# Kernel tuning notes

Hardware: AMD Instinct MI355X
Metric: run time of the kernel (lower is better)

The kernel has to match this reference:

```python
import jax, jax.numpy as jnp
import numpy as np

EPS = 1e-7

def safe_divide(num, den):
    safe_den = jnp.where(jnp.abs(den) > EPS, den, jnp.sign(den) * EPS)
    return num / safe_den

def mlp(x, W1, b1, W2, b2):
    return jnp.tanh(x @ W1 + b1) @ W2 + b2

B, L, C, H, T = 16384, 256, 512, 1024, 16

def setup_inputs() -> dict:
    key = jax.random.key(0)
    ks = jax.random.split(key, 12)
    s = 0.05
    z = jax.random.normal(ks[0], (B, 2 * L + 1), dtype=jnp.float32)
    ctx = jax.random.normal(ks[1], (B, T, C), dtype=jnp.float32)
    ts = jnp.arange(T, dtype=jnp.float32) * 0.1  # sorted time knots
    t = jnp.float32(0.75)                        # solver query time
    inverse_mass = jnp.ones((1, L), dtype=jnp.float32)
    # fixed diffusion = sqrt(2*gamma/beta), gamma=1, beta=1/3 -> sqrt(6)
    diffusion = jnp.full((1, L), np.sqrt(6.0), dtype=jnp.float32)
    # control_network: Linear(2L+C -> H), tanh, Linear(H -> L)
    Wc1 = jax.random.normal(ks[2], (2 * L + C, H), dtype=jnp.float32) * s
    bc1 = jnp.zeros((H,), dtype=jnp.float32)
    Wc2 = jax.random.normal(ks[3], (H, L), dtype=jnp.float32) * s
    bc2 = jnp.zeros((L,), dtype=jnp.float32)
    # h_net (prior drift): Linear(2L -> H), tanh, Linear(H -> L)
    Wh1 = jax.random.normal(ks[4], (2 * L, H), dtype=jnp.float32) * s
    bh1 = jnp.zeros((H,), dtype=jnp.float32)
    Wh2 = jax.random.normal(ks[5], (H, L), dtype=jnp.float32) * s
    bh2 = jnp.zeros((L,), dtype=jnp.float32)
    return {"z": z, "ts": ts, "t": t, "ctx": ctx,
            "inverse_mass": inverse_mass, "diffusion": diffusion,
            "Wc1": Wc1, "bc1": bc1, "Wc2": Wc2, "bc2": bc2,
            "Wh1": Wh1, "bh1": bh1, "Wh2": Wh2, "bh2": bh2}

def reference(z, ts, t, ctx, inverse_mass, diffusion,
              Wc1, bc1, Wc2, bc2, Wh1, bh1, Wh2, bh2):
    # f_and_g_absolute: one drift/diffusion evaluation of the second-order latent SDE
    pm = z[..., :-1]                      # [B, 2L] position+momentum
    momentum = pm[..., pm.shape[-1] // 2:]  # [B, L]
    # context lookup via searchsorted(right) clamped to last knot
    i = jnp.minimum(jnp.searchsorted(ts, t, side='right'), ts.shape[0] - 1)
    position_drift = inverse_mass * momentum                      # [B, L]
    prior_momentum_drift = mlp(pm, Wh1, bh1, Wh2, bh2)            # [B, L]
    posterior_momentum_drift = mlp(
        jnp.concatenate([pm, ctx[:, i]], axis=-1), Wc1, bc1, Wc2, bc2)  # [B, L]
    difference = prior_momentum_drift - posterior_momentum_drift
    momentum_diffusion = jnp.broadcast_to(diffusion, (z.shape[0], diffusion.shape[-1]))
    dkl_drift = jnp.sum(jnp.square(safe_divide(difference, momentum_diffusion)),
                        axis=-1, keepdims=True)                   # [B, 1]
    drift = jnp.concatenate([position_drift, posterior_momentum_drift, dkl_drift], axis=-1)
    diffusion_out = jnp.concatenate(
        [jnp.zeros_like(momentum_diffusion), momentum_diffusion,
         jnp.zeros_like(dkl_drift)], axis=-1)
    return drift, diffusion_out
```

## Files before the change

kernel.cpp:

```cpp
#include <hip/hip_runtime.h>

typedef __attribute__((ext_vector_type(8))) short short8;
typedef __attribute__((ext_vector_type(4))) float f32x4;

#define AS1 __attribute__((address_space(1)))
#define AS3 __attribute__((address_space(3)))

#define NB 16384
#define LDIM 256
#define CDIM 512
#define HDIM 1024

__device__ __forceinline__ unsigned short f2bf(float x) {
    unsigned u = __float_as_uint(x);
    u += 0x7fffu + ((u >> 16) & 1u);
    return (unsigned short)(u >> 16);
}

__device__ __forceinline__ void gld_lds16(const unsigned short* g, unsigned short* l) {
    __builtin_amdgcn_global_load_lds((const AS1 void*)g, (AS3 void*)l, 16, 0, 0);
}

__device__ __forceinline__ float tanh_fast(float x) {
    x = fminf(fmaxf(x, -15.f), 15.f);
    float e = __expf(2.f * x);
    return (e - 1.f) / (e + 1.f);
}

__global__ void build_w(const float* __restrict__ Wc1, const float* __restrict__ bc1,
                        const float* __restrict__ Wc2, const float* __restrict__ bc2,
                        const float* __restrict__ Wh1, const float* __restrict__ bh1,
                        const float* __restrict__ Wh2, const float* __restrict__ bh2,
                        unsigned short* __restrict__ W1T, unsigned short* __restrict__ W2T,
                        float* __restrict__ bias1, float* __restrict__ bias2)
{
    const int R1 = 2048 * 1024;
    const int R2 = R1 + 512 * 1024;
    const int R3 = R2 + 2048;
    const int R4 = R3 + 512;
    int id = blockIdx.x * 256 + threadIdx.x;
    if (id < R1) {
        int n = id >> 10, k = id & 1023;
        float v;
        if (n < 1024) v = Wc1[k * 1024 + n];
        else          v = (k < 512) ? Wh1[k * 1024 + (n - 1024)] : 0.f;
        W1T[id] = f2bf(v);
    } else if (id < R2) {
        int id2 = id - R1;
        int n = id2 >> 10, k = id2 & 1023;
        float v = (n < 256) ? Wc2[k * 256 + n] : Wh2[k * 256 + (n - 256)];
        W2T[id2] = f2bf(v);
    } else if (id < R3) {
        int n = id - R2;
        bias1[n] = (n < 1024) ? bc1[n] : bh1[n - 1024];
    } else if (id < R4) {
        int n = id - R3;
        bias2[n] = (n < 256) ? bc2[n] : bh2[n - 256];
    }
}

__global__ void build_A1(const float* __restrict__ z, const float* __restrict__ ts,
                         const float* __restrict__ t, const float* __restrict__ ctx,
                         unsigned short* __restrict__ A1, float* __restrict__ out)
{
    __shared__ int sh_i;
    if (threadIdx.x == 0) {
        float tv = t[0];
        int c = 0;
        #pragma unroll
        for (int q = 0; q < 16; ++q) c += (ts[q] <= tv) ? 1 : 0;
        sh_i = (c < 15) ? c : 15;
    }
    __syncthreads();
    const int i = sh_i;
    size_t id = (size_t)blockIdx.x * 256 + threadIdx.x;
    int b  = (int)(id >> 7);
    int c0 = ((int)id & 127) << 3;
    short8 v;
    if (c0 < 512) {
        const float* zp = z + (size_t)b * 513 + c0;
        #pragma unroll
        for (int q = 0; q < 8; ++q) v[q] = (short)f2bf(zp[q]);
    } else {
        const f32x4* cp = (const f32x4*)(ctx + ((size_t)b * 16 + i) * 512 + (c0 - 512));
        f32x4 x0 = cp[0], x1 = cp[1];
        #pragma unroll
        for (int q = 0; q < 4; ++q) { v[q] = (short)f2bf(x0[q]); v[4 + q] = (short)f2bf(x1[q]); }
    }
    *(short8*)(A1 + id * 8) = v;
    if (id < NB) {
        out[id * 513 + 512] = 0.f;
        out[(size_t)NB * 513 + id * 513 + 512] = 0.f;
    }
}

__global__ __launch_bounds__(256)
void gemm1(const unsigned short* __restrict__ A, const unsigned short* __restrict__ BT,
           const float* __restrict__ bias, unsigned short* __restrict__ Hout)
{
    __shared__ unsigned short sA[128 * 32];
    __shared__ unsigned short sB[128 * 32];

    const int tid  = threadIdx.x;
    const int lane = tid & 63;
    const int wave = tid >> 6;

    int lin = blockIdx.y * 16 + blockIdx.x;
    lin = (lin & 7) * 256 + (lin >> 3);
    const int ntile = lin & 15;
    const int mtile = lin >> 4;
    const int kdim  = (ntile < 8) ? 1024 : 512;

    const int m0 = mtile * 128;
    const int n0 = ntile * 128;

    const int row0 = tid >> 2,         cb0 = tid & 3;
    const int row1 = (256 + tid) >> 2, cb1 = (256 + tid) & 3;

    const unsigned short* aG0 = A + (size_t)(m0 + row0) * 1024 + cb0 * 8;
    const unsigned short* aG1 = A + (size_t)(m0 + row1) * 1024 + cb1 * 8;
    const unsigned short* bG0 = BT + (size_t)(n0 + row0) * 1024 + cb0 * 8;
    const unsigned short* bG1 = BT + (size_t)(n0 + row1) * 1024 + cb1 * 8;

    unsigned short* sA0 = sA + (size_t)(wave * 64) * 8;
    unsigned short* sA1 = sA + (size_t)(256 + wave * 64) * 8;
    unsigned short* sB0 = sB + (size_t)(wave * 64) * 8;
    unsigned short* sB1 = sB + (size_t)(256 + wave * 64) * 8;

    const int wm = (wave & 1) * 64;
    const int wn = (wave >> 1) * 64;
    const int lr = lane & 15;
    const int kq = (lane >> 4) * 8;

    f32x4 acc[4][4] = {};

    for (int k0 = 0; k0 < kdim; k0 += 32) {
        gld_lds16(aG0 + k0, sA0);
        gld_lds16(aG1 + k0, sA1);
        gld_lds16(bG0 + k0, sB0);
        gld_lds16(bG1 + k0, sB1);
        __syncthreads();

        short8 af[4], bfr[4];
        #pragma unroll
        for (int i = 0; i < 4; ++i)
            af[i] = *(const short8*)&sA[(wm + i * 16 + lr) * 32 + kq];
        #pragma unroll
        for (int i = 0; i < 4; ++i)
            bfr[i] = *(const short8*)&sB[(wn + i * 16 + lr) * 32 + kq];

        #pragma unroll
        for (int i = 0; i < 4; ++i)
            #pragma unroll
            for (int j = 0; j < 4; ++j)
                acc[i][j] = __builtin_amdgcn_mfma_f32_16x16x32_bf16(af[i], bfr[j], acc[i][j], 0, 0, 0);
        __syncthreads();
    }

    const int rquad = (lane >> 4) * 4;
    #pragma unroll
    for (int i = 0; i < 4; ++i) {
        const int gr = m0 + wm + i * 16 + rquad;
        #pragma unroll
        for (int j = 0; j < 4; ++j) {
            const int gc = n0 + wn + j * 16 + lr;
            const float bs = bias[gc];
            #pragma unroll
            for (int r = 0; r < 4; ++r) {
                float x = acc[i][j][r] + bs;
                Hout[(size_t)(gr + r) * 2048 + gc] = f2bf(tanh_fast(x));
            }
        }
    }
}

__global__ __launch_bounds__(256)
void gemm2_fused(const unsigned short* __restrict__ Hm, const unsigned short* __restrict__ W2T,
                 const float* __restrict__ bias2, const float* __restrict__ z,
                 const float* __restrict__ im, const float* __restrict__ dfu,
                 float* __restrict__ out)
{
    __shared__ unsigned short sAp[64 * 32];
    __shared__ unsigned short sAq[64 * 32];
    __shared__ unsigned short sBp[128 * 32];
    __shared__ unsigned short sBq[128 * 32];

    const int tid  = threadIdx.x;
    const int lane = tid & 63;
    const int wave = tid >> 6;

    int lin = blockIdx.y * 2 + blockIdx.x;
    lin = (lin & 7) * 64 + (lin >> 3);
    const int n0 = (lin & 1) * 128;
    const int m0 = (lin >> 1) * 64;

    const int arow = tid >> 2, acb = tid & 3;
    const int brow1 = (256 + tid) >> 2, bcb1 = (256 + tid) & 3;

    const unsigned short* aGp  = Hm  + (size_t)(m0 + arow) * 2048 + acb * 8;
    const unsigned short* aGq  = aGp + 1024;
    const unsigned short* bGp0 = W2T + (size_t)(n0 + arow) * 1024 + acb * 8;
    const unsigned short* bGp1 = W2T + (size_t)(n0 + brow1) * 1024 + bcb1 * 8;
    const unsigned short* bGq0 = bGp0 + 256 * 1024;
    const unsigned short* bGq1 = bGp1 + 256 * 1024;

    unsigned short* dAp  = sAp + wave * 512;
    unsigned short* dAq  = sAq + wave * 512;
    unsigned short* dBp0 = sBp + wave * 512;
    unsigned short* dBp1 = sBp + 2048 + wave * 512;
    unsigned short* dBq0 = sBq + wave * 512;
    unsigned short* dBq1 = sBq + 2048 + wave * 512;

    const int wn = wave * 32;
    const int lr = lane & 15;
    const int kq = (lane >> 4) * 8;

    f32x4 accp[4][2] = {};
    f32x4 accq[4][2] = {};

    for (int k0 = 0; k0 < 1024; k0 += 32) {
        gld_lds16(aGp  + k0, dAp);
        gld_lds16(aGq  + k0, dAq);
        gld_lds16(bGp0 + k0, dBp0);
        gld_lds16(bGp1 + k0, dBp1);
        gld_lds16(bGq0 + k0, dBq0);
        gld_lds16(bGq1 + k0, dBq1);
        __syncthreads();

        short8 afp[4], afq[4], bp[2], bq[2];
        #pragma unroll
        for (int i = 0; i < 4; ++i) {
            afp[i] = *(const short8*)&sAp[(i * 16 + lr) * 32 + kq];
            afq[i] = *(const short8*)&sAq[(i * 16 + lr) * 32 + kq];
        }
        #pragma unroll
        for (int j = 0; j < 2; ++j) {
            bp[j] = *(const short8*)&sBp[(wn + j * 16 + lr) * 32 + kq];
            bq[j] = *(const short8*)&sBq[(wn + j * 16 + lr) * 32 + kq];
        }

        #pragma unroll
        for (int i = 0; i < 4; ++i)
            #pragma unroll
            for (int j = 0; j < 2; ++j) {
                accp[i][j] = __builtin_amdgcn_mfma_f32_16x16x32_bf16(afp[i], bp[j], accp[i][j], 0, 0, 0);
                accq[i][j] = __builtin_amdgcn_mfma_f32_16x16x32_bf16(afq[i], bq[j], accq[i][j], 0, 0, 0);
            }
        __syncthreads();
    }

    const int rquad = (lane >> 4) * 4;
    float bcv[2], bhv[2], dv[2], sdv[2], imv[2];
    #pragma unroll
    for (int j = 0; j < 2; ++j) {
        const int gc = n0 + wn + j * 16 + lr;
        bcv[j] = bias2[gc];
        bhv[j] = bias2[256 + gc];
        float d = dfu[gc];
        dv[j] = d;
        float sgn = (d > 0.f) ? 1.f : ((d < 0.f) ? -1.f : 0.f);
        sdv[j] = (fabsf(d) > 1e-7f) ? d : sgn * 1e-7f;
        imv[j] = im[gc];
    }

    #pragma unroll
    for (int i = 0; i < 4; ++i) {
        #pragma unroll
        for (int r = 0; r < 4; ++r) {
            const int gr = m0 + i * 16 + rquad + r;
            float* drift = out + (size_t)gr * 513;
            float* dif   = out + (size_t)NB * 513 + (size_t)gr * 513;
            float s2 = 0.f;
            #pragma unroll
            for (int j = 0; j < 2; ++j) {
                const int gc = n0 + wn + j * 16 + lr;
                float post = accp[i][j][r] + bcv[j];
                float pri  = accq[i][j][r] + bhv[j];
                drift[256 + gc] = post;
                drift[gc]       = imv[j] * z[(size_t)gr * 513 + 256 + gc];
                dif[gc]         = 0.f;
                dif[256 + gc]   = dv[j];
                float qq = (pri - post) / sdv[j];
                s2 += qq * qq;
            }
            #pragma unroll
            for (int m = 1; m < 16; m <<= 1) s2 += __shfl_xor(s2, m, 64);
            if (lr == 0) atomicAdd(&drift[512], s2);
        }
    }
}

extern "C" void kernel_launch(void* const* d_in, const int* in_sizes, int n_in,
                              void* d_out, int out_size, void* d_ws, size_t ws_size,
                              hipStream_t stream) {
    const float* z    = (const float*)d_in[0];
    const float* ts   = (const float*)d_in[1];
    const float* t    = (const float*)d_in[2];
    const float* ctx  = (const float*)d_in[3];
    const float* im   = (const float*)d_in[4];
    const float* dfu  = (const float*)d_in[5];
    const float* Wc1  = (const float*)d_in[6];
    const float* bc1  = (const float*)d_in[7];
    const float* Wc2  = (const float*)d_in[8];
    const float* bc2  = (const float*)d_in[9];
    const float* Wh1  = (const float*)d_in[10];
    const float* bh1  = (const float*)d_in[11];
    const float* Wh2  = (const float*)d_in[12];
    const float* bh2  = (const float*)d_in[13];

    char* ws = (char*)d_ws;
    unsigned short* A1  = (unsigned short*)(ws);
    unsigned short* H   = (unsigned short*)(ws + 33554432ull);
    unsigned short* W1T = (unsigned short*)(ws + 100663296ull);
    unsigned short* W2T = (unsigned short*)(ws + 104857600ull);
    float*          b1  = (float*)(ws + 105906176ull);
    float*          b2  = (float*)(ws + 105914368ull);

    float* out = (float*)d_out;

    build_w<<<10250, 256, 0, stream>>>(Wc1, bc1, Wc2, bc2, Wh1, bh1, Wh2, bh2, W1T, W2T, b1, b2);
    build_A1<<<8192, 256, 0, stream>>>(z, ts, t, ctx, A1, out);

    dim3 g1(16, 128);
    gemm1<<<g1, 256, 0, stream>>>(A1, W1T, b1, H);

    dim3 g2(2, 256);
    gemm2_fused<<<g2, 256, 0, stream>>>(H, W2T, b2, z, im, dfu, out);
}
```

Baseline: 805.6 us.

## Tile weight transpose through LDS, move passthrough outputs to build_A1, widen gemm2

The weight conversion kernel now transposes 64x64 tiles through shared memory, so both the global reads and the bf16 writes are coalesced instead of strided gathers. The position drift and the constant diffusion outputs are written in build_A1, which already loads z, so gemm2 no longer rereads z or stores those columns. gemm2 now runs 8 waves per block, each owning one 16-column MFMA tile, which halves the accumulators per thread. tanh uses a hardware reciprocal instead of a division, at a small accuracy cost.

```diff
diff --git a/kernel.cpp b/kernel.cpp
--- a/kernel.cpp
+++ b/kernel.cpp
@@ -24,43 +24,71 @@
 __device__ __forceinline__ float tanh_fast(float x) {
     x = fminf(fmaxf(x, -15.f), 15.f);
     float e = __expf(2.f * x);
-    return (e - 1.f) / (e + 1.f);
-}
-
-__global__ void build_w(const float* __restrict__ Wc1, const float* __restrict__ bc1,
-                        const float* __restrict__ Wc2, const float* __restrict__ bc2,
-                        const float* __restrict__ Wh1, const float* __restrict__ bh1,
-                        const float* __restrict__ Wh2, const float* __restrict__ bh2,
-                        unsigned short* __restrict__ W1T, unsigned short* __restrict__ W2T,
-                        float* __restrict__ bias1, float* __restrict__ bias2)
+    return (e - 1.f) * __builtin_amdgcn_rcpf(e + 1.f);
+}
+
+__global__ __launch_bounds__(256)
+void build_w(const float* __restrict__ Wc1, const float* __restrict__ bc1,
+             const float* __restrict__ Wc2, const float* __restrict__ bc2,
+             const float* __restrict__ Wh1, const float* __restrict__ bh1,
+             const float* __restrict__ Wh2, const float* __restrict__ bh2,
+             unsigned short* __restrict__ W1T, unsigned short* __restrict__ W2T,
+             float* __restrict__ bias1, float* __restrict__ bias2)
 {
-    const int R1 = 2048 * 1024;
-    const int R2 = R1 + 512 * 1024;
-    const int R3 = R2 + 2048;
-    const int R4 = R3 + 512;
-    int id = blockIdx.x * 256 + threadIdx.x;
-    if (id < R1) {
-        int n = id >> 10, k = id & 1023;
-        float v;
-        if (n < 1024) v = Wc1[k * 1024 + n];
-        else          v = (k < 512) ? Wh1[k * 1024 + (n - 1024)] : 0.f;
-        W1T[id] = f2bf(v);
-    } else if (id < R2) {
-        int id2 = id - R1;
-        int n = id2 >> 10, k = id2 & 1023;
-        float v = (n < 256) ? Wc2[k * 256 + n] : Wh2[k * 256 + (n - 256)];
-        W2T[id2] = f2bf(v);
-    } else if (id < R3) {
-        int n = id - R2;
-        bias1[n] = (n < 1024) ? bc1[n] : bh1[n - 1024];
-    } else if (id < R4) {
-        int n = id - R3;
-        bias2[n] = (n < 256) ? bc2[n] : bh2[n - 256];
+    __shared__ float s[64][65];
+    const int bid = blockIdx.x;
+    const int tid = threadIdx.x;
+
+    if (bid >= 640) {
+        int id = (bid - 640) * 256 + tid;
+        if (id < 2048)      bias1[id] = (id < 1024) ? bc1[id] : bh1[id - 1024];
+        else if (id < 2560) { int n = id - 2048; bias2[n] = (n < 256) ? bc2[n] : bh2[n - 256]; }
+        return;
+    }
+
+    const int tk = bid & 15;
+    const int k0 = tk * 64;
+    const float* src; int srcStride, n0s, kmax, dn0;
+    unsigned short* dst;
+    if (bid < 512) {
+        const int tn = bid >> 4;
+        dst = W1T; dn0 = tn * 64; srcStride = 1024;
+        if (tn < 16) { src = Wc1; n0s = tn * 64;        kmax = 1024; }
+        else         { src = Wh1; n0s = (tn - 16) * 64; kmax = 512;  }
+    } else {
+        const int tn = (bid - 512) >> 4;
+        dst = W2T; dn0 = tn * 64; srcStride = 256;
+        if (tn < 4) { src = Wc2; n0s = tn * 64;       kmax = 1024; }
+        else        { src = Wh2; n0s = (tn - 4) * 64; kmax = 1024; }
+    }
+
+    #pragma unroll
+    for (int rd = 0; rd < 4; ++rd) {
+        int e = rd * 1024 + tid * 4;
+        int r = e >> 6;
+        int c = e & 63;
+        f32x4 v = {0.f, 0.f, 0.f, 0.f};
+        int k = k0 + r;
+        if (k < kmax) v = *(const f32x4*)(src + (size_t)k * srcStride + n0s + c);
+        s[r][c + 0] = v[0]; s[r][c + 1] = v[1]; s[r][c + 2] = v[2]; s[r][c + 3] = v[3];
+    }
+    __syncthreads();
+
+    #pragma unroll
+    for (int wr = 0; wr < 2; ++wr) {
+        int e = wr * 2048 + tid * 8;
+        int on = e >> 6;
+        int ok = e & 63;
+        short8 o;
+        #pragma unroll
+        for (int j = 0; j < 8; ++j) o[j] = (short)f2bf(s[ok + j][on]);
+        *(short8*)(dst + (size_t)(dn0 + on) * 1024 + k0 + ok) = o;
     }
 }
 
 __global__ void build_A1(const float* __restrict__ z, const float* __restrict__ ts,
                          const float* __restrict__ t, const float* __restrict__ ctx,
+                         const float* __restrict__ im, const float* __restrict__ dfu,
                          unsigned short* __restrict__ A1, float* __restrict__ out)
 {
     __shared__ int sh_i;
@@ -79,8 +107,24 @@
     short8 v;
     if (c0 < 512) {
         const float* zp = z + (size_t)b * 513 + c0;
-        #pragma unroll
-        for (int q = 0; q < 8; ++q) v[q] = (short)f2bf(zp[q]);
+        float zv[8];
+        #pragma unroll
+        for (int q = 0; q < 8; ++q) zv[q] = zp[q];
+        #pragma unroll
+        for (int q = 0; q < 8; ++q) v[q] = (short)f2bf(zv[q]);
+        float* drift = out + (size_t)b * 513;
+        float* dif   = out + (size_t)NB * 513 + (size_t)b * 513;
+        if (c0 < 256) {
+            #pragma unroll
+            for (int q = 0; q < 8; ++q) dif[c0 + q] = 0.f;
+        } else {
+            int mc = c0 - 256;
+            #pragma unroll
+            for (int q = 0; q < 8; ++q) {
+                drift[mc + q] = im[mc + q] * zv[q];
+                dif[c0 + q]   = dfu[mc + q];
+            }
+        }
     } else {
         const f32x4* cp = (const f32x4*)(ctx + ((size_t)b * 16 + i) * 512 + (c0 - 512));
         f32x4 x0 = cp[0], x1 = cp[1];
@@ -174,10 +218,9 @@
     }
 }
 
-__global__ __launch_bounds__(256)
+__global__ __launch_bounds__(512)
 void gemm2_fused(const unsigned short* __restrict__ Hm, const unsigned short* __restrict__ W2T,
-                 const float* __restrict__ bias2, const float* __restrict__ z,
-                 const float* __restrict__ im, const float* __restrict__ dfu,
+                 const float* __restrict__ bias2, const float* __restrict__ dfu,
                  float* __restrict__ out)
 {
     __shared__ unsigned short sAp[64 * 32];
@@ -187,105 +230,75 @@
 
     const int tid  = threadIdx.x;
     const int lane = tid & 63;
-    const int wave = tid >> 6;
+    const int w    = tid >> 6;
 
     int lin = blockIdx.y * 2 + blockIdx.x;
     lin = (lin & 7) * 64 + (lin >> 3);
     const int n0 = (lin & 1) * 128;
     const int m0 = (lin >> 1) * 64;
 
-    const int arow = tid >> 2, acb = tid & 3;
-    const int brow1 = (256 + tid) >> 2, bcb1 = (256 + tid) & 3;
-
-    const unsigned short* aGp  = Hm  + (size_t)(m0 + arow) * 2048 + acb * 8;
-    const unsigned short* aGq  = aGp + 1024;
-    const unsigned short* bGp0 = W2T + (size_t)(n0 + arow) * 1024 + acb * 8;
-    const unsigned short* bGp1 = W2T + (size_t)(n0 + brow1) * 1024 + bcb1 * 8;
-    const unsigned short* bGq0 = bGp0 + 256 * 1024;
-    const unsigned short* bGq1 = bGp1 + 256 * 1024;
-
-    unsigned short* dAp  = sAp + wave * 512;
-    unsigned short* dAq  = sAq + wave * 512;
-    unsigned short* dBp0 = sBp + wave * 512;
-    unsigned short* dBp1 = sBp + 2048 + wave * 512;
-    unsigned short* dBq0 = sBq + wave * 512;
-    unsigned short* dBq1 = sBq + 2048 + wave * 512;
-
-    const int wn = wave * 32;
+    const int srow = lane >> 2;
+    const int cb   = lane & 3;
+    const int aseg = w & 3;
+    const unsigned short* aG = Hm + (size_t)(m0 + aseg * 16 + srow) * 2048
+                                  + ((w >> 2) ? 1024 : 0) + cb * 8;
+    unsigned short* aL = ((w >> 2) ? sAq : sAp) + aseg * 512;
+    const unsigned short* bpG = W2T + (size_t)(n0 + w * 16 + srow) * 1024 + cb * 8;
+    const unsigned short* bqG = bpG + 256 * 1024;
+    unsigned short* bpL = sBp + w * 512;
+    unsigned short* bqL = sBq + w * 512;
+
+    const int wn = w * 16;
     const int lr = lane & 15;
     const int kq = (lane >> 4) * 8;
 
-    f32x4 accp[4][2] = {};
-    f32x4 accq[4][2] = {};
+    f32x4 accp[4] = {};
+    f32x4 accq[4] = {};
 
     for (int k0 = 0; k0 < 1024; k0 += 32) {
-        gld_lds16(aGp  + k0, dAp);
-        gld_lds16(aGq  + k0, dAq);
-        gld_lds16(bGp0 + k0, dBp0);
-        gld_lds16(bGp1 + k0, dBp1);
-        gld_lds16(bGq0 + k0, dBq0);
-        gld_lds16(bGq1 + k0, dBq1);
+        gld_lds16(aG  + k0, aL);
+        gld_lds16(bpG + k0, bpL);
+        gld_lds16(bqG + k0, bqL);
         __syncthreads();
 
-        short8 afp[4], afq[4], bp[2], bq[2];
+        short8 afp[4], afq[4], bp, bq;
         #pragma unroll
         for (int i = 0; i < 4; ++i) {
             afp[i] = *(const short8*)&sAp[(i * 16 + lr) * 32 + kq];
             afq[i] = *(const short8*)&sAq[(i * 16 + lr) * 32 + kq];
         }
-        #pragma unroll
-        for (int j = 0; j < 2; ++j) {
-            bp[j] = *(const short8*)&sBp[(wn + j * 16 + lr) * 32 + kq];
-            bq[j] = *(const short8*)&sBq[(wn + j * 16 + lr) * 32 + kq];
-        }
-
-        #pragma unroll
-        for (int i = 0; i < 4; ++i)
-            #pragma unroll
-            for (int j = 0; j < 2; ++j) {
-                accp[i][j] = __builtin_amdgcn_mfma_f32_16x16x32_bf16(afp[i], bp[j], accp[i][j], 0, 0, 0);
-                accq[i][j] = __builtin_amdgcn_mfma_f32_16x16x32_bf16(afq[i], bq[j], accq[i][j], 0, 0, 0);
-            }
+        bp = *(const short8*)&sBp[(wn + lr) * 32 + kq];
+        bq = *(const short8*)&sBq[(wn + lr) * 32 + kq];
+
+        #pragma unroll
+        for (int i = 0; i < 4; ++i) {
+            accp[i] = __builtin_amdgcn_mfma_f32_16x16x32_bf16(afp[i], bp, accp[i], 0, 0, 0);
+            accq[i] = __builtin_amdgcn_mfma_f32_16x16x32_bf16(afq[i], bq, accq[i], 0, 0, 0);
+        }
         __syncthreads();
     }
 
+    const int gc = n0 + wn + lr;
+    const float bcv = bias2[gc];
+    const float bhv = bias2[256 + gc];
+    float d   = dfu[gc];
+    float sgn = (d > 0.f) ? 1.f : ((d < 0.f) ? -1.f : 0.f);
+    float sd  = (fabsf(d) > 1e-7f) ? d : sgn * 1e-7f;
     const int rquad = (lane >> 4) * 4;
-    float bcv[2], bhv[2], dv[2], sdv[2], imv[2];
-    #pragma unroll
-    for (int j = 0; j < 2; ++j) {
-        const int gc = n0 + wn + j * 16 + lr;
-        bcv[j] = bias2[gc];
-        bhv[j] = bias2[256 + gc];
-        float d = dfu[gc];
-        dv[j] = d;
-        float sgn = (d > 0.f) ? 1.f : ((d < 0.f) ? -1.f : 0.f);
-        sdv[j] = (fabsf(d) > 1e-7f) ? d : sgn * 1e-7f;
-        imv[j] = im[gc];
-    }
 
     #pragma unroll
     for (int i = 0; i < 4; ++i) {
         #pragma unroll
         for (int r = 0; r < 4; ++r) {
             const int gr = m0 + i * 16 + rquad + r;
-            float* drift = out + (size_t)gr * 513;
-            float* dif   = out + (size_t)NB * 513 + (size_t)gr * 513;
-            float s2 = 0.f;
-            #pragma unroll
-            for (int j = 0; j < 2; ++j) {
-                const int gc = n0 + wn + j * 16 + lr;
-                float post = accp[i][j][r] + bcv[j];
-                float pri  = accq[i][j][r] + bhv[j];
-                drift[256 + gc] = post;
-                drift[gc]       = imv[j] * z[(size_t)gr * 513 + 256 + gc];
-                dif[gc]         = 0.f;
-                dif[256 + gc]   = dv[j];
-                float qq = (pri - post) / sdv[j];
-                s2 += qq * qq;
-            }
+            float post = accp[i][r] + bcv;
+            float pri  = accq[i][r] + bhv;
+            out[(size_t)gr * 513 + 256 + gc] = post;
+            float qq = (pri - post) / sd;
+            float s2 = qq * qq;
             #pragma unroll
             for (int m = 1; m < 16; m <<= 1) s2 += __shfl_xor(s2, m, 64);
-            if (lr == 0) atomicAdd(&drift[512], s2);
+            if (lr == 0) atomicAdd(&out[(size_t)gr * 513 + 512], s2);
         }
     }
 }
@@ -318,12 +331,12 @@
 
     float* out = (float*)d_out;
 
-    build_w<<<10250, 256, 0, stream>>>(Wc1, bc1, Wc2, bc2, Wh1, bh1, Wh2, bh2, W1T, W2T, b1, b2);
-    build_A1<<<8192, 256, 0, stream>>>(z, ts, t, ctx, A1, out);
+    build_w<<<650, 256, 0, stream>>>(Wc1, bc1, Wc2, bc2, Wh1, bh1, Wh2, bh2, W1T, W2T, b1, b2);
+    build_A1<<<8192, 256, 0, stream>>>(z, ts, t, ctx, im, dfu, A1, out);
 
     dim3 g1(16, 128);
     gemm1<<<g1, 256, 0, stream>>>(A1, W1T, b1, H);
 
     dim3 g2(2, 256);
-    gemm2_fused<<<g2, 256, 0, stream>>>(H, W2T, b2, z, im, dfu, out);
-}
+    gemm2_fused<<<g2, 512, 0, stream>>>(H, W2T, b2, dfu, out);
+}
```

Result: faster. 773.1 us (-4.0%).
